# Kernel optimization log

Hardware: AMD Instinct MI355X
Metric: run time of the kernel (lower is better)

Reference implementation:

```python
import jax, jax.numpy as jnp
import numpy as np

B, L, H, E, D = 4, 2048, 8, 64, 64  # seq S == L (causal mask requires square scores)


def setup_inputs() -> dict:
    key = jax.random.key(0)
    k0, k1, k2, k3, k4 = jax.random.split(key, 5)
    queries = jax.random.normal(k0, (B, L, H, E), jnp.float32)
    keys = jax.random.normal(k1, (B, L, H, E), jnp.float32)
    values = jax.random.normal(k2, (B, L, H, D), jnp.float32)
    # per-sample learned de-stationary scale (positive) and bias
    tau = jax.random.uniform(k3, (B, 1, 1), jnp.float32, 0.5, 1.5)
    delta = jax.random.normal(k4, (B, 1, L), jnp.float32) * 0.1
    return {"queries": queries, "keys": keys, "values": values, "tau": tau, "delta": delta}


def reference(queries, keys, values, tau, delta):
    Bq, Lq, Hq, Eq = queries.shape
    S = keys.shape[1]
    scale = 1.0 / jnp.sqrt(jnp.asarray(Eq, jnp.float32))
    # torch path: rearrange('b s h d l -> (b d) s h l') with s=h=d=1 -> [B,1,1,1] / [B,1,1,S]
    tau_b = tau.reshape(Bq, 1, 1, 1)
    delta_b = delta.reshape(Bq, 1, 1, -1)[..., :S]
    # scores: [B, H, L, S]
    scores = jnp.einsum('blhe,bshe->bhls', queries, keys) * tau_b + delta_b
    causal = jnp.triu(jnp.ones((Lq, S), bool), k=1)  # True above diagonal -> masked
    scores = jnp.where(causal, -jnp.inf, scores)
    A = jax.nn.softmax(scale * scores, axis=-1)  # dropout is identity in eval/reference
    V = jnp.einsum('bhls,bshd->blhd', A, values)  # [B, L, H, D]
    return V
```

## Files before the change

kernel.cpp:

```cpp
#include <hip/hip_runtime.h>
#include <hip/hip_bf16.h>

#define Bsz 4
#define Lsz 2048
#define Hsz 8

typedef __attribute__((ext_vector_type(8))) short bf16x8;
typedef __attribute__((ext_vector_type(4))) short bf16x4;
typedef __attribute__((ext_vector_type(4))) float f32x4;

__device__ __forceinline__ short f2bs(float f) {
    union { float f; unsigned u; } v; v.f = f;
    unsigned r = v.u + 0x7FFFu + ((v.u >> 16) & 1u);
    return (short)(r >> 16);
}
__device__ __forceinline__ short f2bs_rh(float f) {
    return (short)((__float_as_uint(f) + 0x8000u) >> 16);
}

__device__ __forceinline__ void stage16(const short* g, short* l) {
    __builtin_amdgcn_global_load_lds(
        (const __attribute__((address_space(1))) unsigned int*)g,
        (__attribute__((address_space(3))) unsigned int*)l,
        16, 0, 0);
}

__global__ __launch_bounds__(256) void prep_kv(
    const float* __restrict__ ksrc, const float* __restrict__ vsrc,
    short* __restrict__ Kf, short* __restrict__ Vf)
{
    __shared__ float Tl[64][65];
    const int raw = blockIdx.x;
    const int tid = threadIdx.x;
    const bool isK = raw < Bsz*Hsz*32;
    const int bid = isK ? raw : raw - Bsz*Hsz*32;
    const int tl = bid & 31, bh = bid >> 5;
    const int b = bh >> 3, h = bh & 7;

    const int row = tid >> 2, c0 = (tid & 3) * 16;
    const float* src = (isK ? ksrc : vsrc)
                     + (((size_t)b*Lsz + tl*64 + row)*Hsz + h)*64 + c0;
    *(float4*)&Tl[row][c0]      = *(const float4*)(src);
    *(float4*)&Tl[row][c0 + 4]  = *(const float4*)(src + 4);
    *(float4*)&Tl[row][c0 + 8]  = *(const float4*)(src + 8);
    *(float4*)&Tl[row][c0 + 12] = *(const float4*)(src + 12);
    __syncthreads();

    const int lane = tid & 63, ln = lane & 15, quad = lane >> 4;
    if (isK) {
        short* dst = Kf + (size_t)bid * 4096;
        #pragma unroll
        for (int cc = 0; cc < 2; ++cc) {
            const int c  = (tid >> 6)*2 + cc;
            const int nt = c >> 1, eh = c & 1;
            const float* rp = &Tl[nt*16 + ln][eh*32 + quad*8];
            bf16x8 o = {f2bs(rp[0]),f2bs(rp[1]),f2bs(rp[2]),f2bs(rp[3]),
                        f2bs(rp[4]),f2bs(rp[5]),f2bs(rp[6]),f2bs(rp[7])};
            *(bf16x8*)(dst + c*512 + lane*8) = o;
        }
    } else {
        short* dst = Vf + (size_t)bid * 4096;
        #pragma unroll
        for (int cc = 0; cc < 2; ++cc) {
            const int cp  = (tid >> 6)*2 + cc;
            const int m16 = cp >> 1, nt0 = (cp & 1)*2;
            const int d   = m16*16 + ln;
            const int s0  = nt0*16 + quad*4;
            bf16x8 o = {f2bs(Tl[s0+0][d]),  f2bs(Tl[s0+1][d]),
                        f2bs(Tl[s0+2][d]),  f2bs(Tl[s0+3][d]),
                        f2bs(Tl[s0+16][d]), f2bs(Tl[s0+17][d]),
                        f2bs(Tl[s0+18][d]), f2bs(Tl[s0+19][d])};
            *(bf16x8*)(dst + cp*512 + lane*8) = o;
        }
    }
}

__global__ __launch_bounds__(256, 4) void dsattn_main(
    const float* __restrict__ q,
    const short* __restrict__ Kf,
    const short* __restrict__ Vf,
    const float* __restrict__ tau,
    const float* __restrict__ delta,
    float* __restrict__ out)
{
    __shared__ __align__(16) short Kb[2][4096];
    __shared__ __align__(16) short Vb[2][4096];
    __shared__ float dls[Lsz];

    const int tid  = threadIdx.x;
    const int wv   = tid >> 6;
    const int lane = tid & 63;
    const int ln   = lane & 15;
    const int quad = lane >> 4;

    const int bh = blockIdx.x;
    const int b  = bh >> 3, h = bh & 7;
    const int j  = blockIdx.y, aj = j & 7, gj = j >> 3;
    const int qt = (gj == 0) ? aj : (gj == 1) ? 15 - aj
                 : (gj == 2) ? 16 + aj : 31 - aj;
    const int q0 = qt * 64;
    const int T  = qt + 1;

    const float c2  = 0.125f * 1.44269504f;
    const float st2 = c2 * tau[b];

    const short* kt = Kf + (size_t)bh * (32*4096);
    const short* vt = Vf + (size_t)bh * (32*4096);

    const short* gsrc = ((wv < 2) ? kt : vt) + (wv & 1)*2048 + lane*8;

#define STAGE(buf) do {                                                     \
        short* lb_ = (wv < 2 ? &Kb[(buf)][0] : &Vb[(buf)][0]) + (wv&1)*2048;\
        stage16(gsrc + 0*512, lb_ + 0*512);                                 \
        stage16(gsrc + 1*512, lb_ + 1*512);                                 \
        stage16(gsrc + 2*512, lb_ + 2*512);                                 \
        stage16(gsrc + 3*512, lb_ + 3*512);                                 \
        gsrc += 4096;                                                       \
    } while (0)

    STAGE(0);

    {
        const float* dsrc = delta + (size_t)b*Lsz + tid*8;
        float4 a = *(const float4*)(dsrc);
        float4 c = *(const float4*)(dsrc + 4);
        a.x*=c2; a.y*=c2; a.z*=c2; a.w*=c2;
        c.x*=c2; c.y*=c2; c.z*=c2; c.w*=c2;
        *(float4*)&dls[tid*8]     = a;
        *(float4*)&dls[tid*8 + 4] = c;
    }

    bf16x8 qf0, qf1;
    {
        const float* qrow = q + (((size_t)b*Lsz + q0 + wv*16 + ln)*Hsz + h)*64;
        float4 a0 = *(const float4*)(qrow + quad*8);
        float4 a1 = *(const float4*)(qrow + quad*8 + 4);
        float4 b0 = *(const float4*)(qrow + 32 + quad*8);
        float4 b1 = *(const float4*)(qrow + 32 + quad*8 + 4);
        qf0 = (bf16x8){f2bs(a0.x),f2bs(a0.y),f2bs(a0.z),f2bs(a0.w),
                       f2bs(a1.x),f2bs(a1.y),f2bs(a1.z),f2bs(a1.w)};
        qf1 = (bf16x8){f2bs(b0.x),f2bs(b0.y),f2bs(b0.z),f2bs(b0.w),
                       f2bs(b1.x),f2bs(b1.y),f2bs(b1.z),f2bs(b1.w)};
    }

    f32x4 oacc[4];
    #pragma unroll
    for (int m = 0; m < 4; ++m) oacc[m] = (f32x4){0.f,0.f,0.f,0.f};
    f32x4 sE[4], sO[4];
    bf16x8 vv[8];
    bf16x4 pT[4];
    float l_acc = 0.f;

#define QK(tt, SW) do {                                                     \
        const short* Kc_ = &Kb[(tt)&1][0];                                  \
        _Pragma("unroll")                                                   \
        for (int nt = 0; nt < 4; ++nt) {                                    \
            bf16x8 kf0_ = *(const bf16x8*)(Kc_ + (nt*2+0)*512 + lane*8);    \
            bf16x8 kf1_ = *(const bf16x8*)(Kc_ + (nt*2+1)*512 + lane*8);    \
            f32x4 z_ = (f32x4){0.f,0.f,0.f,0.f};                            \
            z_ = __builtin_amdgcn_mfma_f32_16x16x32_bf16(kf0_, qf0, z_, 0,0,0); \
            (SW)[nt] = __builtin_amdgcn_mfma_f32_16x16x32_bf16(kf1_, qf1, z_, 0,0,0); \
        }                                                                   \
    } while (0)

#define SM(tm, SR) do {                                                     \
        const int k0_ = (tm)*64;                                            \
        _Pragma("unroll")                                                   \
        for (int nt = 0; nt < 4; ++nt) {                                    \
            f32x4 dlv_ = *(const f32x4*)&dls[k0_ + nt*16 + quad*4];         \
            float p0_ = __builtin_amdgcn_exp2f(fmaf((SR)[nt][0], st2, dlv_[0])); \
            float p1_ = __builtin_amdgcn_exp2f(fmaf((SR)[nt][1], st2, dlv_[1])); \
            float p2_ = __builtin_amdgcn_exp2f(fmaf((SR)[nt][2], st2, dlv_[2])); \
            float p3_ = __builtin_amdgcn_exp2f(fmaf((SR)[nt][3], st2, dlv_[3])); \
            l_acc += (p0_ + p1_) + (p2_ + p3_);                             \
            pT[nt] = (bf16x4){f2bs_rh(p0_), f2bs_rh(p1_),                   \
                              f2bs_rh(p2_), f2bs_rh(p3_)};                  \
        }                                                                   \
    } while (0)

#define PV() do {                                                           \
        _Pragma("unroll")                                                   \
        for (int ntp = 0; ntp < 2; ++ntp)                                   \
            _Pragma("unroll")                                               \
            for (int m16 = 0; m16 < 4; ++m16) {                             \
                bf16x8 v8_ = vv[m16*2 + ntp];                               \
                bf16x4 v0_ = (bf16x4){v8_[0], v8_[1], v8_[2], v8_[3]};      \
                bf16x4 v1_ = (bf16x4){v8_[4], v8_[5], v8_[6], v8_[7]};      \
                oacc[m16] = __builtin_amdgcn_mfma_f32_16x16x16bf16_1k(      \
                    v0_, pT[2*ntp+0], oacc[m16], 0,0,0);                    \
                oacc[m16] = __builtin_amdgcn_mfma_f32_16x16x16bf16_1k(      \
                    v1_, pT[2*ntp+1], oacc[m16], 0,0,0);                    \
            }                                                               \
    } while (0)

#define VLOAD(tt) do {                                                      \
        const short* Vc_ = &Vb[(tt)&1][0];                                  \
        _Pragma("unroll")                                                   \
        for (int c = 0; c < 8; ++c)                                         \
            vv[c] = *(const bf16x8*)(Vc_ + c*512 + lane*8);                 \
    } while (0)

#define BODY(tt, SW, SR) do {                                               \
        if ((tt) + 1 < T) STAGE(((tt)+1)&1);                                \
        __builtin_amdgcn_s_setprio(1);                                      \
        QK((tt), SW);                  \
        SM((tt)-1, SR);                \
        PV();                          \
        __builtin_amdgcn_s_setprio(0);                                      \
        VLOAD(tt);                     \
        __syncthreads();                                                    \
    } while (0)

    __syncthreads();

    if (T > 1) STAGE(1);
    __builtin_amdgcn_s_setprio(1);
    QK(0, sE);
    __builtin_amdgcn_s_setprio(0);
    VLOAD(0);
    __syncthreads();

    int t = 1;
    for (; t + 1 < T; t += 2) {
        BODY(t,     sO, sE);
        BODY(t + 1, sE, sO);
    }
    if (t < T) BODY(t, sO, sE);

    if ((T - 1) & 1) {
        #pragma unroll
        for (int nt = 0; nt < 4; ++nt) sE[nt] = sO[nt];
    }

    {
        const int k0 = (T - 1) * 64;
        const int qrow = q0 + wv*16 + ln;
        #pragma unroll
        for (int nt = 0; nt < 4; ++nt)
            #pragma unroll
            for (int r = 0; r < 4; ++r)
                if (k0 + nt*16 + quad*4 + r > qrow) sE[nt][r] = -1e30f;
        SM(T - 1, sE);
        PV();
    }

    float lsum = l_acc;
    lsum += __shfl_xor(lsum, 16, 64);
    lsum += __shfl_xor(lsum, 32, 64);
    const float inv = 1.0f / lsum;
    const int qrow = q0 + wv*16 + ln;
    float* orow = out + (((size_t)b*Lsz + qrow)*Hsz + h)*64;
    #pragma unroll
    for (int m16 = 0; m16 < 4; ++m16) {
        float4 o = {oacc[m16][0]*inv, oacc[m16][1]*inv,
                    oacc[m16][2]*inv, oacc[m16][3]*inv};
        *(float4*)(orow + m16*16 + quad*4) = o;
    }
#undef STAGE
#undef QK
#undef SM
#undef PV
#undef VLOAD
#undef BODY
}

extern "C" void kernel_launch(void* const* d_in, const int* in_sizes, int n_in,
                              void* d_out, int out_size, void* d_ws, size_t ws_size,
                              hipStream_t stream) {
    (void)in_sizes; (void)n_in; (void)out_size; (void)ws_size;
    const float* q     = (const float*)d_in[0];
    const float* k     = (const float*)d_in[1];
    const float* v     = (const float*)d_in[2];
    const float* tau   = (const float*)d_in[3];
    const float* delta = (const float*)d_in[4];
    float* out = (float*)d_out;

    short* Kf = (short*)d_ws;
    short* Vf = (short*)d_ws + (size_t)(4*1024*1024);

    prep_kv<<<dim3(Bsz*Hsz*32*2), dim3(256), 0, stream>>>(k, v, Kf, Vf);
    dsattn_main<<<dim3(Bsz*Hsz, 32), dim3(256), 0, stream>>>(q, Kf, Vf, tau, delta, out);
}
```

Baseline: 125.6 us.

## Switch attention to 32x32x16 MFMA with split-K waves and LDS reduction

Moves both QK and PV from 16x16 MFMA tiles to 32x32x16 bf16 MFMA. Each wave now owns a 32-query by 32-key quadrant, and the two key halves are summed through LDS at the end. P is packed with v_cvt_pk_bf16_f32 and permlane32_swap, which replaces per-element rounding and the old software-pipelined QK/softmax/PV schedule with a simpler per-tile body. The K/V prep layout is changed to match the new fragments and the tile order is reshuffled for load balance. In exchange the kernel loses the cross-tile overlap and adds a final LDS reduction and an extra barrier.

Result: no change. 123.9 us (-1.3%).

```diff
diff --git a/kernel.cpp b/kernel.cpp
--- a/kernel.cpp
+++ b/kernel.cpp
@@ -5,17 +5,20 @@
 #define Lsz 2048
 #define Hsz 8
 
-typedef __attribute__((ext_vector_type(8))) short bf16x8;
-typedef __attribute__((ext_vector_type(4))) short bf16x4;
-typedef __attribute__((ext_vector_type(4))) float f32x4;
+typedef __attribute__((ext_vector_type(8)))  short bf16x8;
+typedef __attribute__((ext_vector_type(4)))  float f32x4;
+typedef __attribute__((ext_vector_type(16))) float f32x16;
+typedef __attribute__((ext_vector_type(2)))  unsigned u32x2;
 
 __device__ __forceinline__ short f2bs(float f) {
     union { float f; unsigned u; } v; v.f = f;
     unsigned r = v.u + 0x7FFFu + ((v.u >> 16) & 1u);
     return (short)(r >> 16);
 }
-__device__ __forceinline__ short f2bs_rh(float f) {
-    return (short)((__float_as_uint(f) + 0x8000u) >> 16);
+__device__ __forceinline__ unsigned cvtpk(float lo, float hi) {
+    unsigned r;
+    asm("v_cvt_pk_bf16_f32 %0, %1, %2" : "=v"(r) : "v"(lo), "v"(hi));
+    return r;
 }
 
 __device__ __forceinline__ void stage16(const short* g, short* l) {
@@ -46,14 +49,14 @@
     *(float4*)&Tl[row][c0 + 12] = *(const float4*)(src + 12);
     __syncthreads();
 
-    const int lane = tid & 63, ln = lane & 15, quad = lane >> 4;
+    const int lane = tid & 63, l31 = lane & 31, hi = lane >> 5;
     if (isK) {
         short* dst = Kf + (size_t)bid * 4096;
         #pragma unroll
         for (int cc = 0; cc < 2; ++cc) {
             const int c  = (tid >> 6)*2 + cc;
-            const int nt = c >> 1, eh = c & 1;
-            const float* rp = &Tl[nt*16 + ln][eh*32 + quad*8];
+            const int kh = c >> 2, eb = c & 3;
+            const float* rp = &Tl[kh*32 + l31][eb*16 + hi*8];
             bf16x8 o = {f2bs(rp[0]),f2bs(rp[1]),f2bs(rp[2]),f2bs(rp[3]),
                         f2bs(rp[4]),f2bs(rp[5]),f2bs(rp[6]),f2bs(rp[7])};
             *(bf16x8*)(dst + c*512 + lane*8) = o;
@@ -62,15 +65,15 @@
         short* dst = Vf + (size_t)bid * 4096;
         #pragma unroll
         for (int cc = 0; cc < 2; ++cc) {
-            const int cp  = (tid >> 6)*2 + cc;
-            const int m16 = cp >> 1, nt0 = (cp & 1)*2;
-            const int d   = m16*16 + ln;
-            const int s0  = nt0*16 + quad*4;
-            bf16x8 o = {f2bs(Tl[s0+0][d]),  f2bs(Tl[s0+1][d]),
-                        f2bs(Tl[s0+2][d]),  f2bs(Tl[s0+3][d]),
-                        f2bs(Tl[s0+16][d]), f2bs(Tl[s0+17][d]),
-                        f2bs(Tl[s0+18][d]), f2bs(Tl[s0+19][d])};
-            *(bf16x8*)(dst + cp*512 + lane*8) = o;
+            const int c  = (tid >> 6)*2 + cc;
+            const int dh = c >> 2, kb = c & 3;
+            const int d  = dh*32 + l31;
+            const int s0 = kb*16 + hi*8;
+            bf16x8 o = {f2bs(Tl[s0+0][d]), f2bs(Tl[s0+1][d]),
+                        f2bs(Tl[s0+2][d]), f2bs(Tl[s0+3][d]),
+                        f2bs(Tl[s0+4][d]), f2bs(Tl[s0+5][d]),
+                        f2bs(Tl[s0+6][d]), f2bs(Tl[s0+7][d])};
+            *(bf16x8*)(dst + c*512 + lane*8) = o;
         }
     }
 }
@@ -90,14 +93,16 @@
     const int tid  = threadIdx.x;
     const int wv   = tid >> 6;
     const int lane = tid & 63;
-    const int ln   = lane & 15;
-    const int quad = lane >> 4;
+    const int l31  = lane & 31;
+    const int hi   = lane >> 5;
+    const int qh   = wv & 1;
+    const int kh   = wv >> 1;
 
     const int bh = blockIdx.x;
     const int b  = bh >> 3, h = bh & 7;
     const int j  = blockIdx.y, aj = j & 7, gj = j >> 3;
-    const int qt = (gj == 0) ? aj : (gj == 1) ? 15 - aj
-                 : (gj == 2) ? 16 + aj : 31 - aj;
+    const int qt = (gj == 0) ? 31 - 2*aj : (gj == 1) ? 30 - 2*aj
+                 : (gj == 2) ? 2*aj + 1  : 2*aj;
     const int q0 = qt * 64;
     const int T  = qt + 1;
 
@@ -130,138 +135,132 @@
         *(float4*)&dls[tid*8 + 4] = c;
     }
 
-    bf16x8 qf0, qf1;
+    bf16x8 qf[4];
     {
-        const float* qrow = q + (((size_t)b*Lsz + q0 + wv*16 + ln)*Hsz + h)*64;
-        float4 a0 = *(const float4*)(qrow + quad*8);
-        float4 a1 = *(const float4*)(qrow + quad*8 + 4);
-        float4 b0 = *(const float4*)(qrow + 32 + quad*8);
-        float4 b1 = *(const float4*)(qrow + 32 + quad*8 + 4);
-        qf0 = (bf16x8){f2bs(a0.x),f2bs(a0.y),f2bs(a0.z),f2bs(a0.w),
-                       f2bs(a1.x),f2bs(a1.y),f2bs(a1.z),f2bs(a1.w)};
-        qf1 = (bf16x8){f2bs(b0.x),f2bs(b0.y),f2bs(b0.z),f2bs(b0.w),
-                       f2bs(b1.x),f2bs(b1.y),f2bs(b1.z),f2bs(b1.w)};
-    }
-
-    f32x4 oacc[4];
+        const float* qrow = q + (((size_t)b*Lsz + q0 + qh*32 + l31)*Hsz + h)*64 + hi*8;
+        #pragma unroll
+        for (int eb = 0; eb < 4; ++eb) {
+            float4 a0 = *(const float4*)(qrow + eb*16);
+            float4 a1 = *(const float4*)(qrow + eb*16 + 4);
+            qf[eb] = (bf16x8){f2bs(a0.x),f2bs(a0.y),f2bs(a0.z),f2bs(a0.w),
+                              f2bs(a1.x),f2bs(a1.y),f2bs(a1.z),f2bs(a1.w)};
+        }
+    }
+
+    f32x16 oacc0, oacc1;
     #pragma unroll
-    for (int m = 0; m < 4; ++m) oacc[m] = (f32x4){0.f,0.f,0.f,0.f};
-    f32x4 sE[4], sO[4];
-    bf16x8 vv[8];
-    bf16x4 pT[4];
+    for (int i = 0; i < 16; ++i) { oacc0[i] = 0.f; oacc1[i] = 0.f; }
     float l_acc = 0.f;
 
-#define QK(tt, SW) do {                                                     \
-        const short* Kc_ = &Kb[(tt)&1][0];                                  \
-        _Pragma("unroll")                                                   \
-        for (int nt = 0; nt < 4; ++nt) {                                    \
-            bf16x8 kf0_ = *(const bf16x8*)(Kc_ + (nt*2+0)*512 + lane*8);    \
-            bf16x8 kf1_ = *(const bf16x8*)(Kc_ + (nt*2+1)*512 + lane*8);    \
-            f32x4 z_ = (f32x4){0.f,0.f,0.f,0.f};                            \
-            z_ = __builtin_amdgcn_mfma_f32_16x16x32_bf16(kf0_, qf0, z_, 0,0,0); \
-            (SW)[nt] = __builtin_amdgcn_mfma_f32_16x16x32_bf16(kf1_, qf1, z_, 0,0,0); \
-        }                                                                   \
+    __syncthreads();
+
+#define TILE_BODY(t_, MASKED) do {                                          \
+        const int cur_ = (t_) & 1;                                          \
+        const short* Kc_ = &Kb[cur_][0];                                    \
+        const short* Vc_ = &Vb[cur_][0];                                    \
+        const int k0_ = (t_)*64;                                            \
+         \
+        f32x16 sacc;                                                        \
+        _Pragma("unroll")                                                   \
+        for (int i = 0; i < 16; ++i) sacc[i] = 0.f;                         \
+        __builtin_amdgcn_s_setprio(1);                                      \
+        _Pragma("unroll")                                                   \
+        for (int eb = 0; eb < 4; ++eb) {                                    \
+            bf16x8 kf_ = *(const bf16x8*)(Kc_ + (kh*4 + eb)*512 + lane*8);  \
+            sacc = __builtin_amdgcn_mfma_f32_32x32x16_bf16(kf_, qf[eb], sacc, 0,0,0); \
+        }                                                                   \
+        __builtin_amdgcn_s_setprio(0);                                      \
+        if (MASKED) {                                                       \
+            const int qrw_ = qh*32 + l31;                                   \
+            _Pragma("unroll")                                               \
+            for (int g = 0; g < 4; ++g)                                     \
+                _Pragma("unroll")                                           \
+                for (int i = 0; i < 4; ++i)                                 \
+                    if (kh*32 + 8*g + 4*hi + i > qrw_) sacc[g*4+i] = -1e30f;\
+        }                                                                   \
+                                           \
+        float p_[16];                                                       \
+        _Pragma("unroll")                                                   \
+        for (int g = 0; g < 4; ++g) {                                       \
+            f32x4 dlv_ = *(const f32x4*)&dls[k0_ + kh*32 + g*8 + hi*4];     \
+            _Pragma("unroll")                                               \
+            for (int i = 0; i < 4; ++i)                                     \
+                p_[g*4+i] = __builtin_amdgcn_exp2f(fmaf(sacc[g*4+i], st2, dlv_[i])); \
+            l_acc += (p_[g*4]+p_[g*4+1]) + (p_[g*4+2]+p_[g*4+3]);           \
+        }                                                                   \
+                \
+        bf16x8 pf_[2];                                                      \
+        _Pragma("unroll")                                                   \
+        for (int kb = 0; kb < 2; ++kb) {                                    \
+            unsigned a0_ = cvtpk(p_[kb*8+0], p_[kb*8+1]);                   \
+            unsigned a1_ = cvtpk(p_[kb*8+2], p_[kb*8+3]);                   \
+            unsigned b0_ = cvtpk(p_[kb*8+4], p_[kb*8+5]);                   \
+            unsigned b1_ = cvtpk(p_[kb*8+6], p_[kb*8+7]);                   \
+            u32x2 s0_ = __builtin_amdgcn_permlane32_swap(a0_, b0_, false, false); \
+            u32x2 s1_ = __builtin_amdgcn_permlane32_swap(a1_, b1_, false, false); \
+            union { unsigned u[4]; bf16x8 v; } pk_;                         \
+            pk_.u[0] = s0_[0]; pk_.u[1] = s1_[0];                           \
+            pk_.u[2] = s0_[1]; pk_.u[3] = s1_[1];                           \
+            pf_[kb] = pk_.v;                                                \
+        }                                                                   \
+                               \
+        __builtin_amdgcn_s_setprio(1);                                      \
+        _Pragma("unroll")                                                   \
+        for (int kb = 0; kb < 2; ++kb) {                                    \
+            bf16x8 vf0_ = *(const bf16x8*)(Vc_ + (     kh*2 + kb)*512 + lane*8); \
+            bf16x8 vf1_ = *(const bf16x8*)(Vc_ + (4 +  kh*2 + kb)*512 + lane*8); \
+            oacc0 = __builtin_amdgcn_mfma_f32_32x32x16_bf16(vf0_, pf_[kb], oacc0, 0,0,0); \
+            oacc1 = __builtin_amdgcn_mfma_f32_32x32x16_bf16(vf1_, pf_[kb], oacc1, 0,0,0); \
+        }                                                                   \
+        __builtin_amdgcn_s_setprio(0);                                      \
     } while (0)
 
-#define SM(tm, SR) do {                                                     \
-        const int k0_ = (tm)*64;                                            \
-        _Pragma("unroll")                                                   \
-        for (int nt = 0; nt < 4; ++nt) {                                    \
-            f32x4 dlv_ = *(const f32x4*)&dls[k0_ + nt*16 + quad*4];         \
-            float p0_ = __builtin_amdgcn_exp2f(fmaf((SR)[nt][0], st2, dlv_[0])); \
-            float p1_ = __builtin_amdgcn_exp2f(fmaf((SR)[nt][1], st2, dlv_[1])); \
-            float p2_ = __builtin_amdgcn_exp2f(fmaf((SR)[nt][2], st2, dlv_[2])); \
-            float p3_ = __builtin_amdgcn_exp2f(fmaf((SR)[nt][3], st2, dlv_[3])); \
-            l_acc += (p0_ + p1_) + (p2_ + p3_);                             \
-            pT[nt] = (bf16x4){f2bs_rh(p0_), f2bs_rh(p1_),                   \
-                              f2bs_rh(p2_), f2bs_rh(p3_)};                  \
-        }                                                                   \
-    } while (0)
-
-#define PV() do {                                                           \
-        _Pragma("unroll")                                                   \
-        for (int ntp = 0; ntp < 2; ++ntp)                                   \
-            _Pragma("unroll")                                               \
-            for (int m16 = 0; m16 < 4; ++m16) {                             \
-                bf16x8 v8_ = vv[m16*2 + ntp];                               \
-                bf16x4 v0_ = (bf16x4){v8_[0], v8_[1], v8_[2], v8_[3]};      \
-                bf16x4 v1_ = (bf16x4){v8_[4], v8_[5], v8_[6], v8_[7]};      \
-                oacc[m16] = __builtin_amdgcn_mfma_f32_16x16x16bf16_1k(      \
-                    v0_, pT[2*ntp+0], oacc[m16], 0,0,0);                    \
-                oacc[m16] = __builtin_amdgcn_mfma_f32_16x16x16bf16_1k(      \
-                    v1_, pT[2*ntp+1], oacc[m16], 0,0,0);                    \
-            }                                                               \
-    } while (0)
-
-#define VLOAD(tt) do {                                                      \
-        const short* Vc_ = &Vb[(tt)&1][0];                                  \
-        _Pragma("unroll")                                                   \
-        for (int c = 0; c < 8; ++c)                                         \
-            vv[c] = *(const bf16x8*)(Vc_ + c*512 + lane*8);                 \
-    } while (0)
-
-#define BODY(tt, SW, SR) do {                                               \
-        if ((tt) + 1 < T) STAGE(((tt)+1)&1);                                \
-        __builtin_amdgcn_s_setprio(1);                                      \
-        QK((tt), SW);                  \
-        SM((tt)-1, SR);                \
-        PV();                          \
-        __builtin_amdgcn_s_setprio(0);                                      \
-        VLOAD(tt);                     \
-        __syncthreads();                                                    \
-    } while (0)
-
-    __syncthreads();
-
-    if (T > 1) STAGE(1);
-    __builtin_amdgcn_s_setprio(1);
-    QK(0, sE);
-    __builtin_amdgcn_s_setprio(0);
-    VLOAD(0);
-    __syncthreads();
-
-    int t = 1;
-    for (; t + 1 < T; t += 2) {
-        BODY(t,     sO, sE);
-        BODY(t + 1, sE, sO);
-    }
-    if (t < T) BODY(t, sO, sE);
-
-    if ((T - 1) & 1) {
-        #pragma unroll
-        for (int nt = 0; nt < 4; ++nt) sE[nt] = sO[nt];
-    }
-
-    {
-        const int k0 = (T - 1) * 64;
-        const int qrow = q0 + wv*16 + ln;
-        #pragma unroll
-        for (int nt = 0; nt < 4; ++nt)
+    for (int t = 0; t + 1 < T; ++t) {
+        STAGE((t + 1) & 1);
+        TILE_BODY(t, false);
+        __syncthreads();
+    }
+    TILE_BODY(T - 1, true);
+
+    float lw = l_acc + __shfl_xor(l_acc, 32, 64);
+    float* Ored = (float*)&Kb[0][0];
+    float* lred = (float*)&Vb[0][0];
+    __syncthreads();
+
+    if (kh == 1) {
+        #pragma unroll
+        for (int g = 0; g < 4; ++g)
             #pragma unroll
-            for (int r = 0; r < 4; ++r)
-                if (k0 + nt*16 + quad*4 + r > qrow) sE[nt][r] = -1e30f;
-        SM(T - 1, sE);
-        PV();
-    }
-
-    float lsum = l_acc;
-    lsum += __shfl_xor(lsum, 16, 64);
-    lsum += __shfl_xor(lsum, 32, 64);
-    const float inv = 1.0f / lsum;
-    const int qrow = q0 + wv*16 + ln;
-    float* orow = out + (((size_t)b*Lsz + qrow)*Hsz + h)*64;
-    #pragma unroll
-    for (int m16 = 0; m16 < 4; ++m16) {
-        float4 o = {oacc[m16][0]*inv, oacc[m16][1]*inv,
-                    oacc[m16][2]*inv, oacc[m16][3]*inv};
-        *(float4*)(orow + m16*16 + quad*4) = o;
+            for (int i = 0; i < 4; ++i) {
+                const int d_ = 8*g + 4*hi + i;
+                Ored[(qh*64 +      d_)*32 + l31] = oacc0[g*4+i];
+                Ored[(qh*64 + 32 + d_)*32 + l31] = oacc1[g*4+i];
+            }
+        if (lane < 32) lred[qh*32 + l31] = lw;
+    }
+    __syncthreads();
+
+    if (kh == 0) {
+        const float invl = 1.0f / (lw + lred[qh*32 + l31]);
+        float* orow = out + (((size_t)b*Lsz + q0 + qh*32 + l31)*Hsz + h)*64;
+        #pragma unroll
+        for (int g = 0; g < 4; ++g) {
+            const int d_ = 8*g + 4*hi;
+            float4 o0, o1;
+            o0.x = (oacc0[g*4+0] + Ored[(qh*64 + d_ + 0)*32 + l31]) * invl;
+            o0.y = (oacc0[g*4+1] + Ored[(qh*64 + d_ + 1)*32 + l31]) * invl;
+            o0.z = (oacc0[g*4+2] + Ored[(qh*64 + d_ + 2)*32 + l31]) * invl;
+            o0.w = (oacc0[g*4+3] + Ored[(qh*64 + d_ + 3)*32 + l31]) * invl;
+            o1.x = (oacc1[g*4+0] + Ored[(qh*64 + 32 + d_ + 0)*32 + l31]) * invl;
+            o1.y = (oacc1[g*4+1] + Ored[(qh*64 + 32 + d_ + 1)*32 + l31]) * invl;
+            o1.z = (oacc1[g*4+2] + Ored[(qh*64 + 32 + d_ + 2)*32 + l31]) * invl;
+            o1.w = (oacc1[g*4+3] + Ored[(qh*64 + 32 + d_ + 3)*32 + l31]) * invl;
+            *(float4*)(orow + d_)      = o0;
+            *(float4*)(orow + 32 + d_) = o1;
+        }
     }
 #undef STAGE
-#undef QK
-#undef SM
-#undef PV
-#undef VLOAD
-#undef BODY
+#undef TILE_BODY
 }
 
 extern "C" void kernel_launch(void* const* d_in, const int* in_sizes, int n_in,
```
